# Kernel optimization log

Measured on AMD Instinct MI355X. Metric: run time of the kernel, lower is better.

Reference implementation:

```python
import jax, jax.numpy as jnp
import numpy as np

B, T, R, D, M = 4, 256, 100, 128, 256

def setup_inputs() -> dict:
    key = jax.random.key(0)
    ks = jax.random.split(key, 12)
    s = 0.02
    return {
        'x': jax.random.normal(ks[0], (B, T, R, D), dtype=jnp.float32),
        'mask': jax.random.randint(ks[1], (B, T), 0, 2).astype(jnp.int32),
        'Wq': jax.random.normal(ks[2], (D, D), dtype=jnp.float32) * s,
        'bq': jnp.zeros((D,), jnp.float32),
        'Wk': jax.random.normal(ks[3], (D, D), dtype=jnp.float32) * s,
        'bk': jnp.zeros((D,), jnp.float32),
        'Wv': jax.random.normal(ks[4], (D, D), dtype=jnp.float32) * s,
        'bv': jnp.zeros((D,), jnp.float32),
        'Wp': jax.random.normal(ks[5], (D, D), dtype=jnp.float32) * s,
        'bp': jnp.zeros((D,), jnp.float32),
        'ln_g': jnp.ones((D,), jnp.float32),
        'ln_b': jnp.zeros((D,), jnp.float32),
        'rel_table': jax.random.normal(ks[6], (2 * M - 1, 1), dtype=jnp.float32) * s,
    }


def reference(x, mask, Wq, bq, Wk, bk, Wv, bv, Wp, bp, ln_g, ln_b, rel_table):
    b, t, r, d = x.shape
    m = (rel_table.shape[0] + 1) // 2  # max_time_steps
    # faithful to torch .view(B*R, T, D): raw row-major reshape (no transpose)
    xr = x.reshape(b * r, t, d)
    q = xr @ Wq + bq
    k = xr @ Wk + bk
    v = xr @ Wv + bv
    scale = jnp.asarray(1.0 / np.sqrt(d), x.dtype)
    s = jnp.einsum('ntd,nsd->nts', q, k) * scale  # [B*R, T, T]
    # relative position bias
    ids = jnp.clip(jnp.arange(t)[:, None] - jnp.arange(t)[None, :] + (m - 1), 0, 2 * m - 2)
    s = s + rel_table[ids, 0][None, :, :]
    # padding mask (key and query sides)
    am = jnp.repeat(mask[:, None, :], r, axis=1).reshape(b * r, t)  # [B*R, T]
    neg = jnp.asarray(-1e9, s.dtype)
    s = jnp.where(am[:, None, :] == 0, neg, s)
    s = jnp.where(am[:, :, None] == 0, neg, s)
    # causal mask
    causal = jnp.triu(jnp.ones((t, t), dtype=bool), 1)
    s = jnp.where(causal[None, :, :], neg, s)
    w = jax.nn.softmax(s, axis=-1)
    ctx = jnp.einsum('nts,nsd->ntd', w, v)
    out = ctx @ Wp + bp
    y = xr + out
    mu = jnp.mean(y, axis=-1, keepdims=True)
    var = jnp.mean((y - mu) ** 2, axis=-1, keepdims=True)
    y = (y - mu) / jnp.sqrt(var + 1e-5) * ln_g + ln_b
    # faithful to torch .view(B, R, T, D).permute(0, 2, 1, 3)
    return y.reshape(b, r, t, d).transpose(0, 2, 1, 3)
```

## Files before the change

### kernel.cpp

```cpp
#include <hip/hip_runtime.h>
#include <hip/hip_bf16.h>
#include <stdint.h>

typedef float f32x4 __attribute__((ext_vector_type(4)));
typedef __bf16 bf16x8 __attribute__((ext_vector_type(8)));
typedef unsigned short u16;

#define MFMA16(a, b, c) __builtin_amdgcn_mfma_f32_16x16x32_bf16((a), (b), (c), 0, 0, 0)

__device__ __forceinline__ u16 f2bf(float f) {
  union { float f; uint32_t u; } v; v.f = f;
  uint32_t u = v.u;
  return (u16)((u + 0x7fffu + ((u >> 16) & 1u)) >> 16);
}
__device__ __forceinline__ float bf2f(u16 h) {
  union { uint32_t u; float f; } v; v.u = ((uint32_t)h) << 16;
  return v.f;
}

__global__ void prep_weights_kernel(const float* __restrict__ Wq, const float* __restrict__ Wk,
                                    const float* __restrict__ Wv, const float* __restrict__ Wp,
                                    u16* __restrict__ Wt) {
  int w = blockIdx.x;
  const float* W = (w == 0) ? Wq : (w == 1) ? Wk : (w == 2) ? Wv : Wp;
  int t = blockIdx.y * 256 + threadIdx.x;
  int c = t >> 7, k = t & 127;
  Wt[(w * 128 + c) * 128 + k] = f2bf(W[k * 128 + c]);
}

__global__ __launch_bounds__(512, 2) void fused10_kernel(
    const u16* __restrict__ Wt, const float* __restrict__ x,
    const int* __restrict__ mask, const float* __restrict__ rel,
    const float* __restrict__ bq, const float* __restrict__ bk,
    const float* __restrict__ bv, const float* __restrict__ bp,
    const float* __restrict__ ln_g, const float* __restrict__ ln_b,
    float* __restrict__ out) {
  __shared__ u16 KX[256][136];
  __shared__ u16 V_lds[128][264];
  __shared__ u16 P_lds[8][32][40];
  __shared__ float rel_lds[511];
  __shared__ float vmean_lds[128];
  const int tid = threadIdx.x;
  const int n = blockIdx.x;
  const int bb = n / 100, rr = n - bb * 100;
  const int* mrow = mask + bb * 256;
  if (tid < 511) rel_lds[tid] = rel[tid];
  const int l = tid & 63, wv = tid >> 6, l15 = l & 15, l4 = l >> 4;
  const int tt0 = wv * 32;

#define LOADW4(buf, ROWB)                                                  \
  do {                                                                     \
    const u16* _wp = Wt + (size_t)((ROWB) + l15) * 128 + l4 * 8;           \
    buf[0] = *(const bf16x8*)(_wp);                                        \
    buf[1] = *(const bf16x8*)(_wp + 32);                                   \
    buf[2] = *(const bf16x8*)(_wp + 64);                                   \
    buf[3] = *(const bf16x8*)(_wp + 96);                                   \
  } while (0)

  bf16x8 bA[4], bB[4];
  LOADW4(bA, 0);

  {
    int row = tt0 + (l >> 1), half = (l & 1) * 64;
    const float* src = x + ((size_t)(n * 256 + row)) * 128 + half;
    u16* dst = &KX[row][half];
    float4 xr[16];
#pragma unroll
    for (int j = 0; j < 16; ++j) xr[j] = ((const float4*)src)[j];
#pragma unroll
    for (int j = 0; j < 16; ++j) {
      dst[j * 4 + 0] = f2bf(xr[j].x); dst[j * 4 + 1] = f2bf(xr[j].y);
      dst[j * 4 + 2] = f2bf(xr[j].z); dst[j * 4 + 3] = f2bf(xr[j].w);
    }
  }
  int ttg[2][4], qm[2][4];
#pragma unroll
  for (int g = 0; g < 2; ++g)
#pragma unroll
    for (int rg = 0; rg < 4; ++rg) {
      ttg[g][rg] = tt0 + g * 16 + 4 * l4 + rg;
      qm[g][rg] = mrow[ttg[g][rg]];
    }

  bf16x8 af[2][4];
#pragma unroll
  for (int g = 0; g < 2; ++g)
#pragma unroll
    for (int ks = 0; ks < 4; ++ks)
      af[g][ks] = *(const bf16x8*)&KX[tt0 + g * 16 + l15][ks * 32 + l4 * 8];
  uint32_t xres[2][4][4];
#pragma unroll
  for (int g = 0; g < 2; ++g)
#pragma unroll
    for (int rg = 0; rg < 4; ++rg) {
      const u16* xr = &KX[tt0 + g * 16 + 4 * l4 + rg][0];
#pragma unroll
      for (int c = 0; c < 4; ++c)
        xres[g][rg][c] = (uint32_t)xr[c * 32 + l15] | ((uint32_t)xr[c * 32 + 16 + l15] << 16);
    }

  const float scale = 0.088388347648318447f;
  f32x4 t0, t1;
#define MF8(buf)                                                           \
  do {                                                                     \
    t0 = f32x4{0.f, 0.f, 0.f, 0.f}; t1 = f32x4{0.f, 0.f, 0.f, 0.f};       \
    _Pragma("unroll") for (int ks = 0; ks < 4; ++ks) {                     \
      t0 = MFMA16(af[0][ks], buf[ks], t0);                                 \
      t1 = MFMA16(af[1][ks], buf[ks], t1);                                 \
    }                                                                      \
  } while (0)

  bf16x8 qa[2][4];
#define QSTORE(CT)                                                         \
  do {                                                                     \
    float bqv = bq[(CT) * 16 + l15];                                       \
    _Pragma("unroll") for (int rg = 0; rg < 4; ++rg) {                     \
      P_lds[wv][4 * l4 + rg][((CT) & 1) * 16 + l15] = f2bf((t0[rg] + bqv) * scale); \
      P_lds[wv][16 + 4 * l4 + rg][((CT) & 1) * 16 + l15] = f2bf((t1[rg] + bqv) * scale); \
    }                                                                      \
    if ((CT) & 1) {                                                        \
      qa[0][(CT) >> 1] = *(const bf16x8*)&P_lds[wv][l15][l4 * 8];          \
      qa[1][(CT) >> 1] = *(const bf16x8*)&P_lds[wv][16 + l15][l4 * 8];     \
    }                                                                      \
  } while (0)
  LOADW4(bB, 16);
  MF8(bA); LOADW4(bA, 2 * 16);        QSTORE(0);
  MF8(bB); LOADW4(bB, 3 * 16);        QSTORE(1);
  MF8(bA); LOADW4(bA, 4 * 16);        QSTORE(2);
  MF8(bB); LOADW4(bB, 5 * 16);        QSTORE(3);
  MF8(bA); LOADW4(bA, 6 * 16);        QSTORE(4);
  MF8(bB); LOADW4(bB, 7 * 16);        QSTORE(5);
  MF8(bA); LOADW4(bA, 128 + wv * 16); QSTORE(6);
  MF8(bB); LOADW4(bB, 256 + wv * 16); QSTORE(7);

  __syncthreads();

  const float bkv = bk[wv * 16 + l15];
  const float bvv = bv[wv * 16 + l15];
  f32x4 kacc[16];
#pragma unroll
  for (int r = 0; r < 16; ++r) {
    bf16x8 xf[4];
#pragma unroll
    for (int ks = 0; ks < 4; ++ks)
      xf[ks] = *(const bf16x8*)&KX[r * 16 + l15][ks * 32 + l4 * 8];
    f32x4 ka = f32x4{0.f, 0.f, 0.f, 0.f};
    f32x4 va = f32x4{0.f, 0.f, 0.f, 0.f};
#pragma unroll
    for (int ks = 0; ks < 4; ++ks) {
      ka = MFMA16(xf[ks], bA[ks], ka);
      va = MFMA16(xf[ks], bB[ks], va);
    }
    kacc[r] = ka;
#pragma unroll
    for (int rg = 0; rg < 4; ++rg)
      V_lds[wv * 16 + l15][r * 16 + 4 * l4 + rg] = f2bf(va[rg] + bvv);
  }
  __syncthreads();
#pragma unroll
  for (int r = 0; r < 16; ++r)
#pragma unroll
    for (int rg = 0; rg < 4; ++rg)
      KX[r * 16 + 4 * l4 + rg][wv * 16 + l15] = f2bf(kacc[r][rg] + bkv);
  __syncthreads();

  {
    int d = tid >> 2, seg = tid & 3;
    const u16* vr = &V_lds[d][seg * 64];
    float s = 0.f;
#pragma unroll
    for (int j = 0; j < 8; ++j) {
      uint4 u = *(const uint4*)(vr + j * 8);
      s += bf2f((u16)(u.x & 0xffff)) + bf2f((u16)(u.x >> 16));
      s += bf2f((u16)(u.y & 0xffff)) + bf2f((u16)(u.y >> 16));
      s += bf2f((u16)(u.z & 0xffff)) + bf2f((u16)(u.z >> 16));
      s += bf2f((u16)(u.w & 0xffff)) + bf2f((u16)(u.w >> 16));
    }
    s += __shfl_xor(s, 1); s += __shfl_xor(s, 2);
    if (seg == 0) vmean_lds[d] = s * (1.f / 256.f);
  }
  float lsum[2][4]; f32x4 cacc[2][8];
#pragma unroll
  for (int g = 0; g < 2; ++g)
#pragma unroll
    for (int rg = 0; rg < 4; ++rg) lsum[g][rg] = 0.f;
#pragma unroll
  for (int g = 0; g < 2; ++g)
#pragma unroll
    for (int ct = 0; ct < 8; ++ct) cacc[g][ct] = f32x4{0.f, 0.f, 0.f, 0.f};
  __syncthreads();

  const int nkv = (wv >> 1) + 1;
  for (int kv = 0; kv < nkv; ++kv) {
    const int s0 = kv * 64;
    f32x4 sacc[2][4];
#pragma unroll
    for (int g = 0; g < 2; ++g)
#pragma unroll
      for (int ct = 0; ct < 4; ++ct) sacc[g][ct] = f32x4{0.f, 0.f, 0.f, 0.f};
#pragma unroll
    for (int ct = 0; ct < 4; ++ct)
#pragma unroll
      for (int ks = 0; ks < 4; ++ks) {
        bf16x8 bfr = *(const bf16x8*)&KX[s0 + ct * 16 + l15][ks * 32 + l4 * 8];
#pragma unroll
        for (int g = 0; g < 2; ++g) sacc[g][ct] = MFMA16(qa[g][ks], bfr, sacc[g][ct]);
      }
    int km[4];
#pragma unroll
    for (int ct = 0; ct < 4; ++ct) km[ct] = mrow[s0 + ct * 16 + l15];
    float p[2][4][4];
#pragma unroll
    for (int g = 0; g < 2; ++g)
#pragma unroll
      for (int ct = 0; ct < 4; ++ct) {
        const int ss = s0 + ct * 16 + l15;
#pragma unroll
        for (int rg = 0; rg < 4; ++rg) {
          float sv = sacc[g][ct][rg] + rel_lds[ttg[g][rg] - ss + 255];
          bool msk = (ss > ttg[g][rg]) | (km[ct] == 0) | (qm[g][rg] == 0);
          sv = msk ? -1.0e9f : sv;
          float pv = __expf(sv);
          p[g][ct][rg] = pv;
          lsum[g][rg] += pv;
        }
      }
#pragma unroll
    for (int c = 0; c < 2; ++c) {
#pragma unroll
      for (int g = 0; g < 2; ++g)
#pragma unroll
        for (int c2 = 0; c2 < 2; ++c2)
#pragma unroll
          for (int rg = 0; rg < 4; ++rg)
            P_lds[wv][g * 16 + 4 * l4 + rg][c2 * 16 + l15] = f2bf(p[g][2 * c + c2][rg]);
      bf16x8 pa[2];
#pragma unroll
      for (int g = 0; g < 2; ++g)
        pa[g] = *(const bf16x8*)&P_lds[wv][g * 16 + l15][l4 * 8];
#pragma unroll
      for (int ct = 0; ct < 8; ++ct) {
        bf16x8 vb = *(const bf16x8*)&V_lds[ct * 16 + l15][s0 + c * 32 + l4 * 8];
#pragma unroll
        for (int g = 0; g < 2; ++g) cacc[g][ct] = MFMA16(pa[g], vb, cacc[g][ct]);
      }
    }
  }
  float li[2][4];
#pragma unroll
  for (int g = 0; g < 2; ++g)
#pragma unroll
    for (int rg = 0; rg < 4; ++rg) {
      float rs = lsum[g][rg];
#pragma unroll
      for (int off = 1; off < 16; off <<= 1) rs += __shfl_xor(rs, off);
      li[g][rg] = rs;
    }
  bf16x8 ca[2][4];
#pragma unroll
  for (int q = 0; q < 4; ++q) {
#pragma unroll
    for (int g = 0; g < 2; ++g)
#pragma unroll
      for (int c2 = 0; c2 < 2; ++c2) {
        int ct = 2 * q + c2;
        float vm = vmean_lds[ct * 16 + l15];
#pragma unroll
        for (int rg = 0; rg < 4; ++rg) {
          float cval = cacc[g][ct][rg] / li[g][rg];
          cval = (qm[g][rg] == 0) ? vm : cval;
          P_lds[wv][g * 16 + 4 * l4 + rg][c2 * 16 + l15] = f2bf(cval);
        }
      }
#pragma unroll
    for (int g = 0; g < 2; ++g)
      ca[g][q] = *(const bf16x8*)&P_lds[wv][g * 16 + l15][l4 * 8];
  }
  f32x4 oacc[2][8];
#define OACC(CT)                                                           \
  do {                                                                     \
    oacc[0][CT] = t0; oacc[1][CT] = t1;                                    \
  } while (0)
#define MF8C(buf)                                                          \
  do {                                                                     \
    t0 = f32x4{0.f, 0.f, 0.f, 0.f}; t1 = f32x4{0.f, 0.f, 0.f, 0.f};       \
    _Pragma("unroll") for (int ks = 0; ks < 4; ++ks) {                     \
      t0 = MFMA16(ca[0][ks], buf[ks], t0);                                 \
      t1 = MFMA16(ca[1][ks], buf[ks], t1);                                 \
    }                                                                      \
  } while (0)
  LOADW4(bA, 384 + 0);
  LOADW4(bB, 384 + 16);
  MF8C(bA); LOADW4(bA, 384 + 2 * 16); OACC(0);
  MF8C(bB); LOADW4(bB, 384 + 3 * 16); OACC(1);
  MF8C(bA); LOADW4(bA, 384 + 4 * 16); OACC(2);
  MF8C(bB); LOADW4(bB, 384 + 5 * 16); OACC(3);
  MF8C(bA); LOADW4(bA, 384 + 6 * 16); OACC(4);
  MF8C(bB); LOADW4(bB, 384 + 7 * 16); OACC(5);
  MF8C(bA);                           OACC(6);
  MF8C(bB);                           OACC(7);

  float bpv[8], gv[8], bt[8];
#pragma unroll
  for (int ct = 0; ct < 8; ++ct) {
    int d = ct * 16 + l15;
    bpv[ct] = bp[d]; gv[ct] = ln_g[d]; bt[ct] = ln_b[d];
  }
#pragma unroll
  for (int g = 0; g < 2; ++g)
#pragma unroll
    for (int rg = 0; rg < 4; ++rg) {
      const int tg = ttg[g][rg];
      float yv[8], sum = 0.f, sq = 0.f;
#pragma unroll
      for (int ct = 0; ct < 8; ++ct) {
        uint32_t pr = xres[g][rg][ct >> 1];
        u16 xh = (ct & 1) ? (u16)(pr >> 16) : (u16)(pr & 0xffff);
        float v = oacc[g][ct][rg] + bpv[ct] + bf2f(xh);
        yv[ct] = v; sum += v; sq += v * v;
      }
#pragma unroll
      for (int off = 1; off < 16; off <<= 1) { sum += __shfl_xor(sum, off); sq += __shfl_xor(sq, off); }
      float mean = sum * (1.f / 128.f);
      float var = sq * (1.f / 128.f) - mean * mean;
      float rstd = rsqrtf(var + 1e-5f);
      float* orow = out + (((size_t)(bb * 256 + tg)) * 100 + rr) * 128;
#pragma unroll
      for (int ct = 0; ct < 8; ++ct)
        orow[ct * 16 + l15] = (yv[ct] - mean) * rstd * gv[ct] + bt[ct];
    }
#undef LOADW4
#undef MF8
#undef MF8C
#undef QSTORE
#undef OACC
}

extern "C" void kernel_launch(void* const* d_in, const int* in_sizes, int n_in,
                              void* d_out, int out_size, void* d_ws, size_t ws_size,
                              hipStream_t stream) {
  const float* x    = (const float*)d_in[0];
  const int*   mask = (const int*)d_in[1];
  const float* Wq   = (const float*)d_in[2];
  const float* bq   = (const float*)d_in[3];
  const float* Wk   = (const float*)d_in[4];
  const float* bk   = (const float*)d_in[5];
  const float* Wv   = (const float*)d_in[6];
  const float* bv   = (const float*)d_in[7];
  const float* Wp   = (const float*)d_in[8];
  const float* bp   = (const float*)d_in[9];
  const float* ln_g = (const float*)d_in[10];
  const float* ln_b = (const float*)d_in[11];
  const float* rel  = (const float*)d_in[12];
  float* out = (float*)d_out;
  u16* Wt = (u16*)d_ws;

  hipLaunchKernelGGL(prep_weights_kernel, dim3(4, 64), dim3(256), 0, stream, Wq, Wk, Wv, Wp, Wt);
  hipLaunchKernelGGL(fused10_kernel, dim3(400), dim3(512), 0, stream,
                     Wt, x, mask, rel, bq, bk, bv, bp, ln_g, ln_b, out);
}
```

Before: 83.61 us.

## Split output projection by output-column slice per wave via shared context buffer

```diff
diff --git a/kernel.cpp b/kernel.cpp
--- a/kernel.cpp
+++ b/kernel.cpp
@@ -28,7 +28,7 @@
   Wt[(w * 128 + c) * 128 + k] = f2bf(W[k * 128 + c]);
 }
 
-__global__ __launch_bounds__(512, 2) void fused10_kernel(
+__global__ __launch_bounds__(512, 2) void fused11_kernel(
     const u16* __restrict__ Wt, const float* __restrict__ x,
     const int* __restrict__ mask, const float* __restrict__ rel,
     const float* __restrict__ bq, const float* __restrict__ bk,
@@ -256,67 +256,58 @@
       for (int off = 1; off < 16; off <<= 1) rs += __shfl_xor(rs, off);
       li[g][rg] = rs;
     }
-  bf16x8 ca[2][4];
-#pragma unroll
-  for (int q = 0; q < 4; ++q) {
-#pragma unroll
-    for (int g = 0; g < 2; ++g)
-#pragma unroll
-      for (int c2 = 0; c2 < 2; ++c2) {
-        int ct = 2 * q + c2;
-        float vm = vmean_lds[ct * 16 + l15];
-#pragma unroll
-        for (int rg = 0; rg < 4; ++rg) {
-          float cval = cacc[g][ct][rg] / li[g][rg];
-          cval = (qm[g][rg] == 0) ? vm : cval;
-          P_lds[wv][g * 16 + 4 * l4 + rg][c2 * 16 + l15] = f2bf(cval);
-        }
-      }
-#pragma unroll
-    for (int g = 0; g < 2; ++g)
-      ca[g][q] = *(const bf16x8*)&P_lds[wv][g * 16 + l15][l4 * 8];
-  }
-  f32x4 oacc[2][8];
-#define OACC(CT)                                                           \
-  do {                                                                     \
-    oacc[0][CT] = t0; oacc[1][CT] = t1;                                    \
-  } while (0)
-#define MF8C(buf)                                                          \
-  do {                                                                     \
-    t0 = f32x4{0.f, 0.f, 0.f, 0.f}; t1 = f32x4{0.f, 0.f, 0.f, 0.f};       \
-    _Pragma("unroll") for (int ks = 0; ks < 4; ++ks) {                     \
-      t0 = MFMA16(ca[0][ks], buf[ks], t0);                                 \
-      t1 = MFMA16(ca[1][ks], buf[ks], t1);                                 \
-    }                                                                      \
-  } while (0)
-  LOADW4(bA, 384 + 0);
-  LOADW4(bB, 384 + 16);
-  MF8C(bA); LOADW4(bA, 384 + 2 * 16); OACC(0);
-  MF8C(bB); LOADW4(bB, 384 + 3 * 16); OACC(1);
-  MF8C(bA); LOADW4(bA, 384 + 4 * 16); OACC(2);
-  MF8C(bB); LOADW4(bB, 384 + 5 * 16); OACC(3);
-  MF8C(bA); LOADW4(bA, 384 + 6 * 16); OACC(4);
-  MF8C(bB); LOADW4(bB, 384 + 7 * 16); OACC(5);
-  MF8C(bA);                           OACC(6);
-  MF8C(bB);                           OACC(7);
-
-  float bpv[8], gv[8], bt[8];
+  __syncthreads();
+
+#pragma unroll
+  for (int g = 0; g < 2; ++g)
+#pragma unroll
+    for (int ct = 0; ct < 8; ++ct) {
+      float vm = vmean_lds[ct * 16 + l15];
+#pragma unroll
+      for (int rg = 0; rg < 4; ++rg) {
+        float cval = cacc[g][ct][rg] / li[g][rg];
+        cval = (qm[g][rg] == 0) ? vm : cval;
+        KX[ttg[g][rg]][ct * 16 + l15] = f2bf(cval);
+      }
+    }
+  __syncthreads();
+
+  u16* ybuf = (u16*)V_lds;
+  LOADW4(bA, 384 + wv * 16);
+  const float bpw = bp[wv * 16 + l15];
+#pragma unroll
+  for (int r = 0; r < 16; ++r) {
+    bf16x8 cf[4];
+#pragma unroll
+    for (int ks = 0; ks < 4; ++ks)
+      cf[ks] = *(const bf16x8*)&KX[r * 16 + l15][ks * 32 + l4 * 8];
+    f32x4 ya = f32x4{0.f, 0.f, 0.f, 0.f};
+#pragma unroll
+    for (int ks = 0; ks < 4; ++ks) ya = MFMA16(cf[ks], bA[ks], ya);
+#pragma unroll
+    for (int rg = 0; rg < 4; ++rg)
+      ybuf[(size_t)(r * 16 + 4 * l4 + rg) * 132 + wv * 16 + l15] = f2bf(ya[rg] + bpw);
+  }
+  __syncthreads();
+
+  float gv[8], bt[8];
 #pragma unroll
   for (int ct = 0; ct < 8; ++ct) {
     int d = ct * 16 + l15;
-    bpv[ct] = bp[d]; gv[ct] = ln_g[d]; bt[ct] = ln_b[d];
+    gv[ct] = ln_g[d]; bt[ct] = ln_b[d];
   }
 #pragma unroll
   for (int g = 0; g < 2; ++g)
 #pragma unroll
     for (int rg = 0; rg < 4; ++rg) {
       const int tg = ttg[g][rg];
+      const u16* yr = ybuf + (size_t)tg * 132;
       float yv[8], sum = 0.f, sq = 0.f;
 #pragma unroll
       for (int ct = 0; ct < 8; ++ct) {
         uint32_t pr = xres[g][rg][ct >> 1];
         u16 xh = (ct & 1) ? (u16)(pr >> 16) : (u16)(pr & 0xffff);
-        float v = oacc[g][ct][rg] + bpv[ct] + bf2f(xh);
+        float v = bf2f(yr[ct * 16 + l15]) + bf2f(xh);
         yv[ct] = v; sum += v; sq += v * v;
       }
 #pragma unroll
@@ -331,9 +322,7 @@
     }
 #undef LOADW4
 #undef MF8
-#undef MF8C
 #undef QSTORE
-#undef OACC
 }
 
 extern "C" void kernel_launch(void* const* d_in, const int* in_sizes, int n_in,
@@ -356,6 +345,6 @@
   u16* Wt = (u16*)d_ws;
 
   hipLaunchKernelGGL(prep_weights_kernel, dim3(4, 64), dim3(256), 0, stream, Wq, Wk, Wv, Wp, Wt);
-  hipLaunchKernelGGL(fused10_kernel, dim3(400), dim3(512), 0, stream,
+  hipLaunchKernelGGL(fused11_kernel, dim3(400), dim3(512), 0, stream,
                      Wt, x, mask, rel, bq, bk, bv, bp, ln_g, ln_b, out);
 }
```

New measurement: 89.15 us. +6.6%, slower.
